# Performance work log

Hardware: AMD Instinct MI355X
Metric: run time of the kernel (lower is better)

## Reference

```python
import jax, jax.numpy as jnp
import numpy as np

N_NODES = 50000
N_EDGES = 800000
IN_CH = 64
HID = 128  # hidden_dim_conv == hidden_dim_readout


def setup_inputs() -> dict:
    key = jax.random.key(0)
    ks = jax.random.split(key, 16)
    x = jax.random.normal(ks[0], (N_NODES, 1, IN_CH), dtype=jnp.float32)
    edge_index = jax.random.randint(ks[1], (2, N_EDGES), 0, N_NODES, dtype=jnp.int64)
    edge_weight = jax.random.uniform(ks[2], (N_EDGES,), dtype=jnp.float32)

    def lin(k, out_d, in_d):
        s = 1.0 / np.sqrt(in_d)
        return jax.random.uniform(k, (out_d, in_d), minval=-s, maxval=s, dtype=jnp.float32)

    params = {
        "W_rel0": lin(ks[3], HID, IN_CH), "b_rel0": jnp.zeros((HID,), jnp.float32),
        "W_root0": lin(ks[4], HID, IN_CH),
        "W_ro0": lin(ks[5], HID, HID), "b_ro0": jnp.zeros((HID,), jnp.float32),
        "W_rel1": lin(ks[6], HID, HID), "b_rel1": jnp.zeros((HID,), jnp.float32),
        "W_root1": lin(ks[7], HID, HID),
        "W_ro1": lin(ks[8], HID, HID), "b_ro1": jnp.zeros((HID,), jnp.float32),
        "W_prd": lin(ks[9], 1, HID), "b_prd": jnp.zeros((1,), jnp.float32),
    }
    return {"dynamic_node_features": x, "edge_index": edge_index, "edge_weight": edge_weight, **params}


def reference(dynamic_node_features, edge_index, edge_weight,
              W_rel0, b_rel0, W_root0, W_ro0, b_ro0,
              W_rel1, b_rel1, W_root1, W_ro1, b_ro1,
              W_prd, b_prd):
    # Dropout layers are identity at inference.
    src, dst = edge_index[0], edge_index[1]
    n = dynamic_node_features.shape[0]
    # in-degree counts for 'mean' aggregation (nodes with no in-edges -> 0 output)
    counts = jax.ops.segment_sum(jnp.ones((edge_weight.shape[0],), edge_weight.dtype), dst, num_segments=n)
    denom = jnp.maximum(counts, 1.0)[:, None]  # [N,1]

    def graph_conv(h, W_rel, b_rel, W_root):
        # PyG GraphConv: lin_rel(mean_j edge_weight_ij * h_j) + lin_root(h_i)
        msg = edge_weight[:, None] * h[src]                       # [E,C]
        agg = jax.ops.segment_sum(msg, dst, num_segments=n) / denom  # [N,C]
        return agg @ W_rel.T + b_rel + h @ W_root.T

    h = dynamic_node_features[:, 0, :]                            # [N,IN_CH]
    h = jax.nn.relu(graph_conv(h, W_rel0, b_rel0, W_root0))
    h = jax.nn.relu(h @ W_ro0.T + b_ro0)                          # readout layer 0
    h = jax.nn.relu(graph_conv(h, W_rel1, b_rel1, W_root1))
    h = jax.nn.relu(h @ W_ro1.T + b_ro1)                          # readout layer 1
    out = h @ W_prd.T + b_prd                                     # [N,1]
    return out[:, None, :]                                        # [N,1,1]
```

## Files before the change

kernel.cpp:

```cpp
#include <hip/hip_runtime.h>
#include <hip/hip_fp16.h>

#define N_NODES 50000
#define N_EDGES 800000
#define IN_CH 64
#define HID 128
#define MAXDEG 64

typedef __attribute__((ext_vector_type(8))) short bf16x8;
typedef __attribute__((ext_vector_type(4))) float f32x4;

__device__ __forceinline__ unsigned pack_split(float v) {
    unsigned u = __float_as_uint(v);
    unsigned hi = (u + 0x7fffu + ((u >> 16) & 1u)) & 0xffff0000u;
    float r = v - __uint_as_float(hi);
    unsigned ur = __float_as_uint(r);
    unsigned lo = ((ur + 0x7fffu + ((ur >> 16) & 1u)) >> 16) & 0xffffu;
    return hi | lo;
}


__global__ __launch_bounds__(256) void count_fill_pack(
    const int* __restrict__ src, const int* __restrict__ dst,
    const float* __restrict__ w, int* __restrict__ cnt, int2* __restrict__ csr, int e,
    const float* __restrict__ x, unsigned* __restrict__ xp, __half* __restrict__ xh, int nx,
    const float* __restrict__ w_rel0, const float* __restrict__ w_root0,
    const float* __restrict__ w_ro0, const float* __restrict__ w_rel1,
    const float* __restrict__ w_root1, const float* __restrict__ w_ro1,
    unsigned short* __restrict__ hi, unsigned short* __restrict__ lo) {
    int tid = blockIdx.x * blockDim.x + threadIdx.x;
    int i8 = tid * 8;
    if (i8 + 7 < e) {
        int4 d0 = *(const int4*)&dst[i8];
        int4 d1 = *(const int4*)&dst[i8 + 4];
        int4 s0 = *(const int4*)&src[i8];
        int4 s1 = *(const int4*)&src[i8 + 4];
        float4 w0 = *(const float4*)&w[i8];
        float4 w1 = *(const float4*)&w[i8 + 4];
        int dd[8] = {d0.x, d0.y, d0.z, d0.w, d1.x, d1.y, d1.z, d1.w};
        int ss[8] = {s0.x, s0.y, s0.z, s0.w, s1.x, s1.y, s1.z, s1.w};
        float ww[8] = {w0.x, w0.y, w0.z, w0.w, w1.x, w1.y, w1.z, w1.w};
        int rr[8];
#pragma unroll
        for (int q = 0; q < 8; ++q) rr[q] = atomicAdd(&cnt[dd[q]], 1);
#pragma unroll
        for (int q = 0; q < 8; ++q) {
            if (rr[q] < MAXDEG) {
                unsigned long long v =
                    ((unsigned long long)(unsigned)__float_as_uint(ww[q]) << 32) | (unsigned)ss[q];
                __builtin_nontemporal_store(
                    v, (unsigned long long*)&csr[(size_t)dd[q] * MAXDEG + rr[q]]);
            }
        }
    } else if (i8 < e) {
        for (int i = i8; i < e; ++i) {
            int d = dst[i];
            int r = atomicAdd(&cnt[d], 1);
            if (r < MAXDEG) {
                unsigned long long v =
                    ((unsigned long long)(unsigned)__float_as_uint(w[i]) << 32) | (unsigned)src[i];
                __builtin_nontemporal_store(
                    v, (unsigned long long*)&csr[(size_t)d * MAXDEG + r]);
            }
        }
    }
    if (tid < nx) {
        float v = x[tid];
        xp[tid] = pack_split(v);
        xh[tid] = __float2half(v);
    }
    if (tid < 81920) {
        const float* srcw;
        int li;
        if (tid < 8192) { srcw = w_rel0; li = tid; }
        else if (tid < 16384) { srcw = w_root0; li = tid - 8192; }
        else if (tid < 32768) { srcw = w_ro0; li = tid - 16384; }
        else if (tid < 49152) { srcw = w_rel1; li = tid - 32768; }
        else if (tid < 65536) { srcw = w_root1; li = tid - 49152; }
        else { srcw = w_ro1; li = tid - 65536; }
        unsigned p = pack_split(srcw[li]);
        hi[tid] = (unsigned short)(p >> 16);
        lo[tid] = (unsigned short)(p & 0xffffu);
    }
}


__global__ void aggregate64(const __half2* __restrict__ xh2, const int* __restrict__ cnt,
                            const int2* __restrict__ csr,
                            unsigned* __restrict__ agg, int n) {
    int tid = blockIdx.x * blockDim.x + threadIdx.x;
    int lane = tid & 63;
    int sl = lane & 31;
    int node = ((tid >> 6) << 1) + (lane >> 5);
    if (node >= n) return;
    int deg = cnt[node];
    int end = deg < MAXDEG ? deg : MAXDEG;
    float inv = 1.0f / fmaxf((float)deg, 1.0f);
    const int2* cp = csr + (size_t)node * MAXDEG;
    float ax = 0.0f, ay = 0.0f;
    int e = 0;
    for (; e + 16 <= end; e += 16) {
        int2 p[16];
        __half2 v[16];
#pragma unroll
        for (int q = 0; q < 16; ++q) p[q] = cp[e + q];
#pragma unroll
        for (int q = 0; q < 16; ++q) v[q] = xh2[(size_t)p[q].x * 32 + sl];
#pragma unroll
        for (int q = 0; q < 16; ++q) {
            float wv = __int_as_float(p[q].y);
            float2 f = __half22float2(v[q]);
            ax += wv * f.x;
            ay += wv * f.y;
        }
    }
    for (; e + 4 <= end; e += 4) {
        int2 p[4];
        __half2 v[4];
#pragma unroll
        for (int q = 0; q < 4; ++q) p[q] = cp[e + q];
#pragma unroll
        for (int q = 0; q < 4; ++q) v[q] = xh2[(size_t)p[q].x * 32 + sl];
#pragma unroll
        for (int q = 0; q < 4; ++q) {
            float wv = __int_as_float(p[q].y);
            float2 f = __half22float2(v[q]);
            ax += wv * f.x;
            ay += wv * f.y;
        }
    }
    for (; e < end; ++e) {
        int2 p = cp[e];
        float wv = __int_as_float(p.y);
        float2 f = __half22float2(xh2[(size_t)p.x * 32 + sl]);
        ax += wv * f.x;
        ay += wv * f.y;
    }
    uint2 o;
    o.x = pack_split(ax * inv);
    o.y = pack_split(ay * inv);
    ((uint2*)agg)[(size_t)node * 32 + sl] = o;
}

__global__ void aggregate128(const uint2* __restrict__ h2h, const int* __restrict__ cnt,
                             const int2* __restrict__ csr,
                             unsigned* __restrict__ agg, int n) {
    int tid = blockIdx.x * blockDim.x + threadIdx.x;
    int lane = tid & 63;
    int sl = lane & 31;
    int node = ((tid >> 6) << 1) + (lane >> 5);
    if (node >= n) return;
    int deg = cnt[node];
    int end = deg < MAXDEG ? deg : MAXDEG;
    float inv = 1.0f / fmaxf((float)deg, 1.0f);
    const int2* cp = csr + (size_t)node * MAXDEG;
    float ax = 0.0f, ay = 0.0f, az = 0.0f, aw = 0.0f;
    int e = 0;
    for (; e + 8 <= end; e += 8) {
        int2 p[8];
        uint2 v[8];
#pragma unroll
        for (int q = 0; q < 8; ++q) p[q] = cp[e + q];
#pragma unroll
        for (int q = 0; q < 8; ++q) v[q] = h2h[(size_t)p[q].x * 32 + sl];
#pragma unroll
        for (int q = 0; q < 8; ++q) {
            float wv = __int_as_float(p[q].y);
            float2 f0 = __half22float2(*(const __half2*)&v[q].x);
            float2 f1 = __half22float2(*(const __half2*)&v[q].y);
            ax += wv * f0.x;
            ay += wv * f0.y;
            az += wv * f1.x;
            aw += wv * f1.y;
        }
    }
    for (; e < end; ++e) {
        int2 p = cp[e];
        float wv = __int_as_float(p.y);
        uint2 v = h2h[(size_t)p.x * 32 + sl];
        float2 f0 = __half22float2(*(const __half2*)&v.x);
        float2 f1 = __half22float2(*(const __half2*)&v.y);
        ax += wv * f0.x;
        ay += wv * f0.y;
        az += wv * f1.x;
        aw += wv * f1.y;
    }
    uint4 o;
    o.x = pack_split(ax * inv);
    o.y = pack_split(ay * inv);
    o.z = pack_split(az * inv);
    o.w = pack_split(aw * inv);
    *(uint4*)&agg[(size_t)node * 128 + sl * 4] = o;
}


template <int K1, int NMAT, int EMIT2>
__global__ __launch_bounds__(256) void gemm_fused(
    const unsigned* __restrict__ A0,
    const unsigned short* __restrict__ W0Hi, const unsigned short* __restrict__ W0Lo,
    const unsigned* __restrict__ A1,
    const unsigned short* __restrict__ W1Hi, const unsigned short* __restrict__ W1Lo,
    const float* __restrict__ bias1,
    const unsigned short* __restrict__ W2Hi, const unsigned short* __restrict__ W2Lo,
    const float* __restrict__ bias2,
    void* __restrict__ Yv, __half* __restrict__ Yh,
    const float* __restrict__ pred_w, const float* __restrict__ pred_b,
    float* __restrict__ pred_out, int n) {
    constexpr int KS1 = K1 / 32;
    constexpr int KS2 = 128 / 32;
    const int lane = (int)threadIdx.x & 63;
    const int wv = (int)threadIdx.x >> 6;
    const int col = lane & 15;
    const int quad = lane >> 4;

    __shared__ unsigned h1s[16][132];
    __shared__ float pp[4][16];

    bf16x8 wh1[NMAT][2][KS1], wl1[NMAT][2][KS1];
#pragma unroll
    for (int m = 0; m < NMAT; ++m) {
        const unsigned short* Whi = m ? W1Hi : W0Hi;
        const unsigned short* Wlo = m ? W1Lo : W0Lo;
#pragma unroll
        for (int tt = 0; tt < 2; ++tt) {
            const int j = (2 * wv + tt) * 16 + col;
#pragma unroll
            for (int ks = 0; ks < KS1; ++ks) {
                const size_t wo = (size_t)j * K1 + ks * 32 + quad * 8;
                wh1[m][tt][ks] = *(const bf16x8*)&Whi[wo];
                wl1[m][tt][ks] = *(const bf16x8*)&Wlo[wo];
            }
        }
    }
    bf16x8 wh2[2][KS2], wl2[2][KS2];
#pragma unroll
    for (int tt = 0; tt < 2; ++tt) {
        const int j = (2 * wv + tt) * 16 + col;
#pragma unroll
        for (int ks = 0; ks < KS2; ++ks) {
            const size_t wo = (size_t)j * 128 + ks * 32 + quad * 8;
            wh2[tt][ks] = *(const bf16x8*)&W2Hi[wo];
            wl2[tt][ks] = *(const bf16x8*)&W2Lo[wo];
        }
    }

    float bb1[2], bb2[2], wpv[2];
#pragma unroll
    for (int tt = 0; tt < 2; ++tt) {
        bb1[tt] = bias1[(2 * wv + tt) * 16 + col];
        bb2[tt] = bias2[(2 * wv + tt) * 16 + col];
        if constexpr (EMIT2 == 2) wpv[tt] = pred_w[(2 * wv + tt) * 16 + col];
    }

    const int ngroups = (n + 15) >> 4;
    for (int g = (int)blockIdx.x; g < ngroups; g += (int)gridDim.x) {
        const int m0 = g * 16;
        int arow = m0 + col;
        if (arow >= n) arow = n - 1;

        f32x4 acc[2];
#pragma unroll
        for (int tt = 0; tt < 2; ++tt) acc[tt] = (f32x4){0.f, 0.f, 0.f, 0.f};
#pragma unroll
        for (int m = 0; m < NMAT; ++m) {
            const unsigned* Ap = m ? A1 : A0;
#pragma unroll
            for (int ks = 0; ks < KS1; ++ks) {
                const unsigned* ap = &Ap[(size_t)arow * K1 + ks * 32 + quad * 8];
                uint4 q0 = *(const uint4*)ap;
                uint4 q1 = *(const uint4*)(ap + 4);
                bf16x8 ahi, alo;
                ahi[0] = (short)(q0.x >> 16); alo[0] = (short)(q0.x & 0xffffu);
                ahi[1] = (short)(q0.y >> 16); alo[1] = (short)(q0.y & 0xffffu);
                ahi[2] = (short)(q0.z >> 16); alo[2] = (short)(q0.z & 0xffffu);
                ahi[3] = (short)(q0.w >> 16); alo[3] = (short)(q0.w & 0xffffu);
                ahi[4] = (short)(q1.x >> 16); alo[4] = (short)(q1.x & 0xffffu);
                ahi[5] = (short)(q1.y >> 16); alo[5] = (short)(q1.y & 0xffffu);
                ahi[6] = (short)(q1.z >> 16); alo[6] = (short)(q1.z & 0xffffu);
                ahi[7] = (short)(q1.w >> 16); alo[7] = (short)(q1.w & 0xffffu);
#pragma unroll
                for (int tt = 0; tt < 2; ++tt) {
                    acc[tt] = __builtin_amdgcn_mfma_f32_16x16x32_bf16(ahi, wh1[m][tt][ks], acc[tt], 0, 0, 0);
                    acc[tt] = __builtin_amdgcn_mfma_f32_16x16x32_bf16(ahi, wl1[m][tt][ks], acc[tt], 0, 0, 0);
                    acc[tt] = __builtin_amdgcn_mfma_f32_16x16x32_bf16(alo, wh1[m][tt][ks], acc[tt], 0, 0, 0);
                }
            }
        }
#pragma unroll
        for (int tt = 0; tt < 2; ++tt)
#pragma unroll
            for (int r = 0; r < 4; ++r) {
                float y = fmaxf(acc[tt][r] + bb1[tt], 0.f);
                h1s[quad * 4 + r][(2 * wv + tt) * 16 + col] = pack_split(y);
            }
        __syncthreads();

        f32x4 acc2[2];
#pragma unroll
        for (int tt = 0; tt < 2; ++tt) acc2[tt] = (f32x4){0.f, 0.f, 0.f, 0.f};
#pragma unroll
        for (int ks = 0; ks < KS2; ++ks) {
            const uint4* lp = (const uint4*)&h1s[col][ks * 32 + quad * 8];
            uint4 q0 = lp[0];
            uint4 q1 = lp[1];
            bf16x8 ahi, alo;
            ahi[0] = (short)(q0.x >> 16); alo[0] = (short)(q0.x & 0xffffu);
            ahi[1] = (short)(q0.y >> 16); alo[1] = (short)(q0.y & 0xffffu);
            ahi[2] = (short)(q0.z >> 16); alo[2] = (short)(q0.z & 0xffffu);
            ahi[3] = (short)(q0.w >> 16); alo[3] = (short)(q0.w & 0xffffu);
            ahi[4] = (short)(q1.x >> 16); alo[4] = (short)(q1.x & 0xffffu);
            ahi[5] = (short)(q1.y >> 16); alo[5] = (short)(q1.y & 0xffffu);
            ahi[6] = (short)(q1.z >> 16); alo[6] = (short)(q1.z & 0xffffu);
            ahi[7] = (short)(q1.w >> 16); alo[7] = (short)(q1.w & 0xffffu);
#pragma unroll
            for (int tt = 0; tt < 2; ++tt) {
                acc2[tt] = __builtin_amdgcn_mfma_f32_16x16x32_bf16(ahi, wh2[tt][ks], acc2[tt], 0, 0, 0);
                acc2[tt] = __builtin_amdgcn_mfma_f32_16x16x32_bf16(ahi, wl2[tt][ks], acc2[tt], 0, 0, 0);
                acc2[tt] = __builtin_amdgcn_mfma_f32_16x16x32_bf16(alo, wh2[tt][ks], acc2[tt], 0, 0, 0);
            }
        }

        float yv[2][4];
#pragma unroll
        for (int tt = 0; tt < 2; ++tt)
#pragma unroll
            for (int r = 0; r < 4; ++r)
                yv[tt][r] = fmaxf(acc2[tt][r] + bb2[tt], 0.f);

        if constexpr (EMIT2 == 1) {
#pragma unroll
            for (int tt = 0; tt < 2; ++tt) {
                const int j = (2 * wv + tt) * 16 + col;
#pragma unroll
                for (int r = 0; r < 4; ++r) {
                    int node = m0 + quad * 4 + r;
                    if (node >= n) continue;
                    ((unsigned*)Yv)[(size_t)node * 128 + j] = pack_split(yv[tt][r]);
                    Yh[(size_t)node * 128 + j] = __float2half(yv[tt][r]);
                }
            }
        } else {
            float pr[4];
#pragma unroll
            for (int r = 0; r < 4; ++r) pr[r] = yv[0][r] * wpv[0] + yv[1][r] * wpv[1];
#pragma unroll
            for (int off = 8; off > 0; off >>= 1)
#pragma unroll
                for (int r = 0; r < 4; ++r) pr[r] += __shfl_down(pr[r], off);
            if (col == 0) {
#pragma unroll
                for (int r = 0; r < 4; ++r) pp[wv][quad * 4 + r] = pr[r];
            }
            __syncthreads();
            if (wv == 0 && lane < 16) {
                int node = m0 + lane;
                if (node < n)
                    pred_out[node] = pp[0][lane] + pp[1][lane] + pp[2][lane] + pp[3][lane] + pred_b[0];
            }
        }
        __syncthreads();
    }
}


extern "C" void kernel_launch(void* const* d_in, const int* in_sizes, int n_in,
                              void* d_out, int out_size, void* d_ws, size_t ws_size,
                              hipStream_t stream) {
    const float* x = (const float*)d_in[0];
    const int* edge_index = (const int*)d_in[1];
    const float* edge_w = (const float*)d_in[2];
    const float* W_rel0 = (const float*)d_in[3];
    const float* b_rel0 = (const float*)d_in[4];
    const float* W_root0 = (const float*)d_in[5];
    const float* W_ro0 = (const float*)d_in[6];
    const float* b_ro0 = (const float*)d_in[7];
    const float* W_rel1 = (const float*)d_in[8];
    const float* b_rel1 = (const float*)d_in[9];
    const float* W_root1 = (const float*)d_in[10];
    const float* W_ro1 = (const float*)d_in[11];
    const float* b_ro1 = (const float*)d_in[12];
    const float* W_prd = (const float*)d_in[13];
    const float* b_prd = (const float*)d_in[14];
    float* out = (float*)d_out;

    const int* e_src = edge_index;
    const int* e_dst = edge_index + N_EDGES;

    char* ws = (char*)d_ws;
    size_t off = 0;
    auto alloc = [&](size_t bytes) {
        char* p = ws + off;
        off += (bytes + 255) & ~(size_t)255;
        return p;
    };
    int* cnt = (int*)alloc(N_NODES * 4);
    int2* csr = (int2*)alloc((size_t)N_NODES * MAXDEG * 8);
    unsigned short* WHI = (unsigned short*)alloc(81920 * 2);
    unsigned short* WLO = (unsigned short*)alloc(81920 * 2);
    unsigned* xp = (unsigned*)alloc((size_t)N_NODES * 64 * 4);
    __half* xh = (__half*)alloc((size_t)N_NODES * 64 * 2);
    unsigned* AGGp = (unsigned*)alloc((size_t)N_NODES * 128 * 4);
    unsigned* B2p = (unsigned*)alloc((size_t)N_NODES * 128 * 4);
    __half* H2h = (__half*)alloc((size_t)N_NODES * 128 * 2);

    hipMemsetAsync(cnt, 0, N_NODES * 4, stream);

    const int NX = N_NODES * 64;
    count_fill_pack<<<(NX + 255) / 256, 256, 0, stream>>>(
        e_src, e_dst, edge_w, cnt, csr, N_EDGES,
        x, xp, xh, NX, W_rel0, W_root0, W_ro0, W_rel1, W_root1, W_ro1, WHI, WLO);

    const int AGGB2 = (((N_NODES + 1) / 2) * 64 + 255) / 256;
    const int GGRID = 512;

    aggregate64<<<AGGB2, 256, 0, stream>>>((const __half2*)xh, cnt, csr, AGGp, N_NODES);
    gemm_fused<64, 2, 1><<<GGRID, 256, 0, stream>>>(
        AGGp, WHI + 0, WLO + 0, xp, WHI + 8192, WLO + 8192, b_rel0,
        WHI + 16384, WLO + 16384, b_ro0,
        B2p, H2h, nullptr, nullptr, nullptr, N_NODES);
    aggregate128<<<AGGB2, 256, 0, stream>>>((const uint2*)H2h, cnt, csr, AGGp, N_NODES);
    gemm_fused<128, 2, 2><<<GGRID, 256, 0, stream>>>(
        AGGp, WHI + 32768, WLO + 32768, B2p, WHI + 49152, WLO + 49152, b_rel1,
        WHI + 65536, WLO + 65536, b_ro1,
        nullptr, nullptr, W_prd, b_prd, out, N_NODES);
}
```

Baseline: 279.4 us.

## Use fp16 root-path MFMA and partition CSR fill by destination chunk

The root-term GEMM now reads the existing fp16 copies of x and h (xh/H2h) and runs two f16 MFMAs against split fp16 weights, replacing three bf16 MFMAs on split-bf16 packed fp32 activations. This removes the packed xp and B2p buffers and their writes. The edge fill is restructured so each of 8 block classes only handles destinations in one node chunk, which improves atomic and CSR-write locality but makes every class re-read the whole dst array. The x-to-half conversion is vectorized, and using fp16 activations on the root path lowers its precision.

```diff
diff --git a/kernel.cpp b/kernel.cpp
--- a/kernel.cpp
+++ b/kernel.cpp
@@ -6,8 +6,10 @@
 #define IN_CH 64
 #define HID 128
 #define MAXDEG 64
+#define CHUNK 6250
 
 typedef __attribute__((ext_vector_type(8))) short bf16x8;
+typedef __attribute__((ext_vector_type(8))) _Float16 f16x8;
 typedef __attribute__((ext_vector_type(4))) float f32x4;
 
 __device__ __forceinline__ unsigned pack_split(float v) {
@@ -23,52 +25,39 @@
 __global__ __launch_bounds__(256) void count_fill_pack(
     const int* __restrict__ src, const int* __restrict__ dst,
     const float* __restrict__ w, int* __restrict__ cnt, int2* __restrict__ csr, int e,
-    const float* __restrict__ x, unsigned* __restrict__ xp, __half* __restrict__ xh, int nx,
+    const float* __restrict__ x, __half* __restrict__ xh, int nx,
     const float* __restrict__ w_rel0, const float* __restrict__ w_root0,
     const float* __restrict__ w_ro0, const float* __restrict__ w_rel1,
     const float* __restrict__ w_root1, const float* __restrict__ w_ro1,
-    unsigned short* __restrict__ hi, unsigned short* __restrict__ lo) {
-    int tid = blockIdx.x * blockDim.x + threadIdx.x;
-    int i8 = tid * 8;
-    if (i8 + 7 < e) {
-        int4 d0 = *(const int4*)&dst[i8];
-        int4 d1 = *(const int4*)&dst[i8 + 4];
-        int4 s0 = *(const int4*)&src[i8];
-        int4 s1 = *(const int4*)&src[i8 + 4];
-        float4 w0 = *(const float4*)&w[i8];
-        float4 w1 = *(const float4*)&w[i8 + 4];
-        int dd[8] = {d0.x, d0.y, d0.z, d0.w, d1.x, d1.y, d1.z, d1.w};
-        int ss[8] = {s0.x, s0.y, s0.z, s0.w, s1.x, s1.y, s1.z, s1.w};
-        float ww[8] = {w0.x, w0.y, w0.z, w0.w, w1.x, w1.y, w1.z, w1.w};
-        int rr[8];
-#pragma unroll
-        for (int q = 0; q < 8; ++q) rr[q] = atomicAdd(&cnt[dd[q]], 1);
-#pragma unroll
-        for (int q = 0; q < 8; ++q) {
-            if (rr[q] < MAXDEG) {
-                unsigned long long v =
-                    ((unsigned long long)(unsigned)__float_as_uint(ww[q]) << 32) | (unsigned)ss[q];
-                __builtin_nontemporal_store(
-                    v, (unsigned long long*)&csr[(size_t)dd[q] * MAXDEG + rr[q]]);
-            }
-        }
-    } else if (i8 < e) {
-        for (int i = i8; i < e; ++i) {
-            int d = dst[i];
-            int r = atomicAdd(&cnt[d], 1);
-            if (r < MAXDEG) {
-                unsigned long long v =
-                    ((unsigned long long)(unsigned)__float_as_uint(w[i]) << 32) | (unsigned)src[i];
-                __builtin_nontemporal_store(
-                    v, (unsigned long long*)&csr[(size_t)d * MAXDEG + r]);
-            }
-        }
-    }
-    if (tid < nx) {
-        float v = x[tid];
-        xp[tid] = pack_split(v);
-        xh[tid] = __float2half(v);
-    }
+    unsigned short* __restrict__ hi, unsigned short* __restrict__ lo,
+    unsigned short* __restrict__ rhi, unsigned short* __restrict__ rlo) {
+    const int cls = (int)blockIdx.x & 7;
+    const int slice = (int)blockIdx.x >> 3;
+    const int nsl = (int)gridDim.x >> 3;
+    const int tid = (int)(blockIdx.x * blockDim.x + threadIdx.x);
+
+    for (int i = slice * 256 + (int)threadIdx.x; i < e; i += nsl * 256) {
+        int d = dst[i];
+        if (d / CHUNK != cls) continue;
+        int r = atomicAdd(&cnt[d], 1);
+        if (r < MAXDEG) {
+            unsigned long long v =
+                ((unsigned long long)(unsigned)__float_as_uint(w[i]) << 32) | (unsigned)src[i];
+            __builtin_nontemporal_store(v, (unsigned long long*)&csr[(size_t)d * MAXDEG + r]);
+        }
+    }
+
+    int i4 = tid * 4;
+    if (i4 + 3 < nx) {
+        float4 v = *(const float4*)&x[i4];
+        __half2 a = __floats2half2_rn(v.x, v.y);
+        __half2 b = __floats2half2_rn(v.z, v.w);
+        uint2 o;
+        o.x = *(unsigned*)&a;
+        o.y = *(unsigned*)&b;
+        *(uint2*)&xh[i4] = o;
+    }
+
     if (tid < 81920) {
         const float* srcw;
         int li;
@@ -81,6 +70,20 @@
         unsigned p = pack_split(srcw[li]);
         hi[tid] = (unsigned short)(p >> 16);
         lo[tid] = (unsigned short)(p & 0xffffu);
+    } else if (tid < 90112) {
+        int li = tid - 81920;
+        float v = w_root0[li];
+        __half h = __float2half(v);
+        __half l = __float2half(v - __half2float(h));
+        rhi[li] = __half_as_ushort(h);
+        rlo[li] = __half_as_ushort(l);
+    } else if (tid < 106496) {
+        int li = tid - 90112;
+        float v = w_root1[li];
+        __half h = __float2half(v);
+        __half l = __float2half(v - __half2float(h));
+        rhi[8192 + li] = __half_as_ushort(h);
+        rlo[8192 + li] = __half_as_ushort(l);
     }
 }
 
@@ -194,16 +197,16 @@
 }
 
 
-template <int K1, int NMAT, int EMIT2>
+template <int K1, int EMIT2>
 __global__ __launch_bounds__(256) void gemm_fused(
     const unsigned* __restrict__ A0,
     const unsigned short* __restrict__ W0Hi, const unsigned short* __restrict__ W0Lo,
-    const unsigned* __restrict__ A1,
-    const unsigned short* __restrict__ W1Hi, const unsigned short* __restrict__ W1Lo,
+    const __half* __restrict__ A1h,
+    const unsigned short* __restrict__ W1fHi, const unsigned short* __restrict__ W1fLo,
     const float* __restrict__ bias1,
     const unsigned short* __restrict__ W2Hi, const unsigned short* __restrict__ W2Lo,
     const float* __restrict__ bias2,
-    void* __restrict__ Yv, __half* __restrict__ Yh,
+    __half* __restrict__ Yh,
     const float* __restrict__ pred_w, const float* __restrict__ pred_b,
     float* __restrict__ pred_out, int n) {
     constexpr int KS1 = K1 / 32;
@@ -216,26 +219,20 @@
     __shared__ unsigned h1s[16][132];
     __shared__ float pp[4][16];
 
-    bf16x8 wh1[NMAT][2][KS1], wl1[NMAT][2][KS1];
-#pragma unroll
-    for (int m = 0; m < NMAT; ++m) {
-        const unsigned short* Whi = m ? W1Hi : W0Hi;
-        const unsigned short* Wlo = m ? W1Lo : W0Lo;
-#pragma unroll
-        for (int tt = 0; tt < 2; ++tt) {
-            const int j = (2 * wv + tt) * 16 + col;
-#pragma unroll
-            for (int ks = 0; ks < KS1; ++ks) {
-                const size_t wo = (size_t)j * K1 + ks * 32 + quad * 8;
-                wh1[m][tt][ks] = *(const bf16x8*)&Whi[wo];
-                wl1[m][tt][ks] = *(const bf16x8*)&Wlo[wo];
-            }
-        }
-    }
+    bf16x8 wh1[2][KS1], wl1[2][KS1];
+    f16x8 wf1h[2][KS1], wf1l[2][KS1];
     bf16x8 wh2[2][KS2], wl2[2][KS2];
 #pragma unroll
     for (int tt = 0; tt < 2; ++tt) {
         const int j = (2 * wv + tt) * 16 + col;
+#pragma unroll
+        for (int ks = 0; ks < KS1; ++ks) {
+            const size_t wo = (size_t)j * K1 + ks * 32 + quad * 8;
+            wh1[tt][ks] = *(const bf16x8*)&W0Hi[wo];
+            wl1[tt][ks] = *(const bf16x8*)&W0Lo[wo];
+            wf1h[tt][ks] = *(const f16x8*)&W1fHi[wo];
+            wf1l[tt][ks] = *(const f16x8*)&W1fLo[wo];
+        }
 #pragma unroll
         for (int ks = 0; ks < KS2; ++ks) {
             const size_t wo = (size_t)j * 128 + ks * 32 + quad * 8;
@@ -262,28 +259,33 @@
 #pragma unroll
         for (int tt = 0; tt < 2; ++tt) acc[tt] = (f32x4){0.f, 0.f, 0.f, 0.f};
 #pragma unroll
-        for (int m = 0; m < NMAT; ++m) {
-            const unsigned* Ap = m ? A1 : A0;
-#pragma unroll
-            for (int ks = 0; ks < KS1; ++ks) {
-                const unsigned* ap = &Ap[(size_t)arow * K1 + ks * 32 + quad * 8];
-                uint4 q0 = *(const uint4*)ap;
-                uint4 q1 = *(const uint4*)(ap + 4);
-                bf16x8 ahi, alo;
-                ahi[0] = (short)(q0.x >> 16); alo[0] = (short)(q0.x & 0xffffu);
-                ahi[1] = (short)(q0.y >> 16); alo[1] = (short)(q0.y & 0xffffu);
-                ahi[2] = (short)(q0.z >> 16); alo[2] = (short)(q0.z & 0xffffu);
-                ahi[3] = (short)(q0.w >> 16); alo[3] = (short)(q0.w & 0xffffu);
-                ahi[4] = (short)(q1.x >> 16); alo[4] = (short)(q1.x & 0xffffu);
-                ahi[5] = (short)(q1.y >> 16); alo[5] = (short)(q1.y & 0xffffu);
-                ahi[6] = (short)(q1.z >> 16); alo[6] = (short)(q1.z & 0xffffu);
-                ahi[7] = (short)(q1.w >> 16); alo[7] = (short)(q1.w & 0xffffu);
-#pragma unroll
-                for (int tt = 0; tt < 2; ++tt) {
-                    acc[tt] = __builtin_amdgcn_mfma_f32_16x16x32_bf16(ahi, wh1[m][tt][ks], acc[tt], 0, 0, 0);
-                    acc[tt] = __builtin_amdgcn_mfma_f32_16x16x32_bf16(ahi, wl1[m][tt][ks], acc[tt], 0, 0, 0);
-                    acc[tt] = __builtin_amdgcn_mfma_f32_16x16x32_bf16(alo, wh1[m][tt][ks], acc[tt], 0, 0, 0);
-                }
+        for (int ks = 0; ks < KS1; ++ks) {
+            const unsigned* ap = &A0[(size_t)arow * K1 + ks * 32 + quad * 8];
+            uint4 q0 = *(const uint4*)ap;
+            uint4 q1 = *(const uint4*)(ap + 4);
+            bf16x8 ahi, alo;
+            ahi[0] = (short)(q0.x >> 16); alo[0] = (short)(q0.x & 0xffffu);
+            ahi[1] = (short)(q0.y >> 16); alo[1] = (short)(q0.y & 0xffffu);
+            ahi[2] = (short)(q0.z >> 16); alo[2] = (short)(q0.z & 0xffffu);
+            ahi[3] = (short)(q0.w >> 16); alo[3] = (short)(q0.w & 0xffffu);
+            ahi[4] = (short)(q1.x >> 16); alo[4] = (short)(q1.x & 0xffffu);
+            ahi[5] = (short)(q1.y >> 16); alo[5] = (short)(q1.y & 0xffffu);
+            ahi[6] = (short)(q1.z >> 16); alo[6] = (short)(q1.z & 0xffffu);
+            ahi[7] = (short)(q1.w >> 16); alo[7] = (short)(q1.w & 0xffffu);
+#pragma unroll
+            for (int tt = 0; tt < 2; ++tt) {
+                acc[tt] = __builtin_amdgcn_mfma_f32_16x16x32_bf16(ahi, wh1[tt][ks], acc[tt], 0, 0, 0);
+                acc[tt] = __builtin_amdgcn_mfma_f32_16x16x32_bf16(ahi, wl1[tt][ks], acc[tt], 0, 0, 0);
+                acc[tt] = __builtin_amdgcn_mfma_f32_16x16x32_bf16(alo, wh1[tt][ks], acc[tt], 0, 0, 0);
+            }
+        }
+#pragma unroll
+        for (int ks = 0; ks < KS1; ++ks) {
+            f16x8 af = *(const f16x8*)&A1h[(size_t)arow * K1 + ks * 32 + quad * 8];
+#pragma unroll
+            for (int tt = 0; tt < 2; ++tt) {
+                acc[tt] = __builtin_amdgcn_mfma_f32_16x16x32_f16(af, wf1h[tt][ks], acc[tt], 0, 0, 0);
+                acc[tt] = __builtin_amdgcn_mfma_f32_16x16x32_f16(af, wf1l[tt][ks], acc[tt], 0, 0, 0);
             }
         }
 #pragma unroll
@@ -335,7 +337,6 @@
                 for (int r = 0; r < 4; ++r) {
                     int node = m0 + quad * 4 + r;
                     if (node >= n) continue;
-                    ((unsigned*)Yv)[(size_t)node * 128 + j] = pack_split(yv[tt][r]);
                     Yh[(size_t)node * 128 + j] = __float2half(yv[tt][r]);
                 }
             }
@@ -397,30 +398,30 @@
     int2* csr = (int2*)alloc((size_t)N_NODES * MAXDEG * 8);
     unsigned short* WHI = (unsigned short*)alloc(81920 * 2);
     unsigned short* WLO = (unsigned short*)alloc(81920 * 2);
-    unsigned* xp = (unsigned*)alloc((size_t)N_NODES * 64 * 4);
+    unsigned short* RHI = (unsigned short*)alloc(24576 * 2);
+    unsigned short* RLO = (unsigned short*)alloc(24576 * 2);
     __half* xh = (__half*)alloc((size_t)N_NODES * 64 * 2);
     unsigned* AGGp = (unsigned*)alloc((size_t)N_NODES * 128 * 4);
-    unsigned* B2p = (unsigned*)alloc((size_t)N_NODES * 128 * 4);
     __half* H2h = (__half*)alloc((size_t)N_NODES * 128 * 2);
 
     hipMemsetAsync(cnt, 0, N_NODES * 4, stream);
 
     const int NX = N_NODES * 64;
-    count_fill_pack<<<(NX + 255) / 256, 256, 0, stream>>>(
+    count_fill_pack<<<3200, 256, 0, stream>>>(
         e_src, e_dst, edge_w, cnt, csr, N_EDGES,
-        x, xp, xh, NX, W_rel0, W_root0, W_ro0, W_rel1, W_root1, W_ro1, WHI, WLO);
+        x, xh, NX, W_rel0, W_root0, W_ro0, W_rel1, W_root1, W_ro1, WHI, WLO, RHI, RLO);
 
     const int AGGB2 = (((N_NODES + 1) / 2) * 64 + 255) / 256;
     const int GGRID = 512;
 
     aggregate64<<<AGGB2, 256, 0, stream>>>((const __half2*)xh, cnt, csr, AGGp, N_NODES);
-    gemm_fused<64, 2, 1><<<GGRID, 256, 0, stream>>>(
-        AGGp, WHI + 0, WLO + 0, xp, WHI + 8192, WLO + 8192, b_rel0,
+    gemm_fused<64, 1><<<GGRID, 256, 0, stream>>>(
+        AGGp, WHI + 0, WLO + 0, xh, RHI + 0, RLO + 0, b_rel0,
         WHI + 16384, WLO + 16384, b_ro0,
-        B2p, H2h, nullptr, nullptr, nullptr, N_NODES);
+        H2h, nullptr, nullptr, nullptr, N_NODES);
     aggregate128<<<AGGB2, 256, 0, stream>>>((const uint2*)H2h, cnt, csr, AGGp, N_NODES);
-    gemm_fused<128, 2, 2><<<GGRID, 256, 0, stream>>>(
-        AGGp, WHI + 32768, WLO + 32768, B2p, WHI + 49152, WLO + 49152, b_rel1,
+    gemm_fused<128, 2><<<GGRID, 256, 0, stream>>>(
+        AGGp, WHI + 32768, WLO + 32768, H2h, RHI + 8192, RLO + 8192, b_rel1,
         WHI + 65536, WLO + 65536, b_ro1,
-        nullptr, nullptr, W_prd, b_prd, out, N_NODES);
-}
+        nullptr, W_prd, b_prd, out, N_NODES);
+}
```

Result: faster. 252.8 us (-9.5%).
